# Performance work log

Measured on AMD Instinct MI355X. Metric: run time of the kernel, lower is better.

Reference implementation:

```python
import jax, jax.numpy as jnp
import numpy as np

B, T, I, H = 512, 1024, 64, 128

def setup_inputs() -> dict:
    key = jax.random.key(0)
    ks = jax.random.split(key, 7)
    s_ih = 1.0 / np.sqrt(H)  # torch nn.RNN init scale (uniform +-1/sqrt(H)); use scaled normal for stability
    return {
        "x": jax.random.normal(ks[0], (B, T, I), dtype=jnp.float32),
        "W_ih": jax.random.uniform(ks[1], (H, I), minval=-s_ih, maxval=s_ih, dtype=jnp.float32),
        "W_hh": jax.random.uniform(ks[2], (H, H), minval=-s_ih, maxval=s_ih, dtype=jnp.float32),
        "b_ih": jax.random.uniform(ks[3], (H,), minval=-s_ih, maxval=s_ih, dtype=jnp.float32),
        "b_hh": jax.random.uniform(ks[4], (H,), minval=-s_ih, maxval=s_ih, dtype=jnp.float32),
        "fc_w": jax.random.uniform(ks[5], (1, H), minval=-s_ih, maxval=s_ih, dtype=jnp.float32),
        "fc_b": jax.random.uniform(ks[6], (1,), minval=-s_ih, maxval=s_ih, dtype=jnp.float32),
    }

def reference(x, W_ih, W_hh, b_ih, b_hh, fc_w, fc_b):
    # Precompute input projection for all timesteps in one big GEMM: [B,T,H]
    xp = jnp.einsum("bti,hi->bth", x, W_ih) + b_ih + b_hh
    h0 = jnp.zeros((x.shape[0], W_hh.shape[0]), dtype=x.dtype)

    def step(h, xp_t):
        h = jnp.tanh(xp_t + h @ W_hh.T)
        return h, None

    # scan over time axis; only the final hidden state is needed (out[:, -1, :])
    h_last, _ = jax.lax.scan(step, h0, jnp.swapaxes(xp, 0, 1))
    out = h_last @ fc_w.T + fc_b  # [B, 1]
    return jax.nn.sigmoid(out)
```

## Files before the change

### kernel.cpp

```cpp
#include <hip/hip_runtime.h>


#define Bsz 512
#define Tt  1024
#define Ii  64
#define Hh  128
constexpr int TC = 32;
constexpr int NT = 256;

typedef _Float16 half2v __attribute__((ext_vector_type(2)));
typedef _Float16 half4v __attribute__((ext_vector_type(4)));
typedef _Float16 half8v __attribute__((ext_vector_type(8)));

union h8u { half8v v; half2v h[4]; };

__device__ __forceinline__ float dot2(half2v a, half2v b, float c) {
#if __has_builtin(__builtin_amdgcn_fdot2)
    return __builtin_amdgcn_fdot2(a, b, c, false);
#else
    return c + (float)a[0] * (float)b[0] + (float)a[1] * (float)b[1];
#endif
}

__device__ __forceinline__ float fast_tanh(float x) {
    float t = __builtin_amdgcn_exp2f(x * 2.8853900817779268f);
    return 1.0f - 2.0f * __builtin_amdgcn_rcpf(t + 1.0f);
}
__device__ __forceinline__ float fast_sigmoid(float z) {
    float t = __builtin_amdgcn_exp2f(-z * 1.4426950408889634f);
    return __builtin_amdgcn_rcpf(1.0f + t);
}
__device__ __forceinline__ half4v cvt4(float4 p) {
    half4v r; r[0] = (_Float16)p.x; r[1] = (_Float16)p.y;
    r[2] = (_Float16)p.z; r[3] = (_Float16)p.w; return r;
}

__global__ __launch_bounds__(NT, 4)
void rnn_fused(const float* __restrict__ x,
               const float* __restrict__ W_ih,
               const float* __restrict__ W_hh,
               const float* __restrict__ b_ih,
               const float* __restrict__ b_hh,
               const float* __restrict__ fc_w,
               const float* __restrict__ fc_b,
               float* __restrict__ out)
{
    __shared__ __align__(16) _Float16 xs[2][TC * Ii];
    __shared__ __align__(16) _Float16 hbuf[2][Hh];
    __shared__ float wred[NT / 64];

    const int tid = threadIdx.x;
    const int kq  = tid & 3;
    const int jg  = tid >> 2;
    const int j0  = jg * 2, j1 = j0 + 1;
    const int row = blockIdx.x;

    half2v wih0[8], wih1[8];
    {
        const float* g0 = W_ih + j0 * Ii + kq * 16;
        const float* g1 = W_ih + j1 * Ii + kq * 16;
        #pragma unroll
        for (int k = 0; k < 8; ++k) {
            wih0[k][0] = (_Float16)g0[2*k]; wih0[k][1] = (_Float16)g0[2*k+1];
            wih1[k][0] = (_Float16)g1[2*k]; wih1[k][1] = (_Float16)g1[2*k+1];
        }
    }
    half2v whh0[16], whh1[16];
    {
        const float* g0 = W_hh + j0 * Hh + kq * 32;
        const float* g1 = W_hh + j1 * Hh + kq * 32;
        #pragma unroll
        for (int k = 0; k < 16; ++k) {
            whh0[k][0] = (_Float16)g0[2*k]; whh0[k][1] = (_Float16)g0[2*k+1];
            whh1[k][0] = (_Float16)g1[2*k]; whh1[k][1] = (_Float16)g1[2*k+1];
        }
    }
    const float bias0 = b_ih[j0] + b_hh[j0];
    const float bias1 = b_ih[j1] + b_hh[j1];
    const float fw0 = fc_w[j0], fw1 = fc_w[j1];

    if (tid < Hh / 2) ((half2v*)hbuf[0])[tid] = (half2v)0;

    const float4* xsrc = (const float4*)(x + (size_t)row * Tt * Ii);
    float4 p0 = xsrc[tid];
    float4 p1 = xsrc[tid + NT];

    int   cur = 0;
    float h0n = 0.0f, h1n = 0.0f;

    for (int t0 = 0; t0 < Tt; t0 += TC) {
        const int cbuf = (t0 / TC) & 1;
        ((half4v*)xs[cbuf])[tid]      = cvt4(p0);
        ((half4v*)xs[cbuf])[tid + NT] = cvt4(p1);
        if (t0 + TC < Tt) {
            const int base = (t0 + TC) * (Ii / 4);
            p0 = xsrc[base + tid];
            p1 = xsrc[base + tid + NT];
        }
        __syncthreads();

        #pragma unroll 2
        for (int tt = 0; tt < TC; ++tt) {
            const half8v* xv = (const half8v*)(xs[cbuf] + tt * Ii) + kq * 2;
            const half8v* hv = (const half8v*)(hbuf[cur]) + kq * 4;
            h8u xq0, xq1, hq0, hq1, hq2, hq3;
            xq0.v = xv[0]; xq1.v = xv[1];
            hq0.v = hv[0]; hq1.v = hv[1];
            hq2.v = hv[2]; hq3.v = hv[3];

            float a0 = 0.f, a1 = 0.f, a2 = 0.f, a3 = 0.f;
            float c0 = 0.f, c1 = 0.f, c2 = 0.f, c3 = 0.f;
            #pragma unroll
            for (int k = 0; k < 4; ++k) {
                half2v u0 = xq0.h[k], u1 = xq1.h[k];
                a0 = dot2(u0, wih0[k],     a0);
                a1 = dot2(u1, wih0[k + 4], a1);
                c0 = dot2(u0, wih1[k],     c0);
                c1 = dot2(u1, wih1[k + 4], c1);
            }
            #pragma unroll
            for (int k = 0; k < 4; ++k) {
                half2v v0 = hq0.h[k], v1 = hq1.h[k];
                half2v v2 = hq2.h[k], v3 = hq3.h[k];
                a0 = dot2(v0, whh0[k],      a0);
                a1 = dot2(v1, whh0[k + 4],  a1);
                a2 = dot2(v2, whh0[k + 8],  a2);
                a3 = dot2(v3, whh0[k + 12], a3);
                c0 = dot2(v0, whh1[k],      c0);
                c1 = dot2(v1, whh1[k + 4],  c1);
                c2 = dot2(v2, whh1[k + 8],  c2);
                c3 = dot2(v3, whh1[k + 12], c3);
            }
            float pp0 = (a0 + a1) + (a2 + a3);
            float pp1 = (c0 + c1) + (c2 + c3);
            pp0 += __shfl_xor(pp0, 1, 64);
            pp0 += __shfl_xor(pp0, 2, 64);
            pp1 += __shfl_xor(pp1, 1, 64);
            pp1 += __shfl_xor(pp1, 2, 64);
            h0n = fast_tanh(pp0 + bias0);
            h1n = fast_tanh(pp1 + bias1);
            if (kq == 0) {
                half2v hw; hw[0] = (_Float16)h0n; hw[1] = (_Float16)h1n;
                ((half2v*)hbuf[cur ^ 1])[jg] = hw;
            }
            __syncthreads();
            cur ^= 1;
        }
    }

    float partial = (kq == 0) ? (fw0 * h0n + fw1 * h1n) : 0.0f;
    #pragma unroll
    for (int off = 32; off > 0; off >>= 1)
        partial += __shfl_down(partial, off, 64);
    if ((tid & 63) == 0) wred[tid >> 6] = partial;
    __syncthreads();
    if (tid == 0) {
        float z = fc_b[0];
        #pragma unroll
        for (int w = 0; w < NT / 64; ++w) z += wred[w];
        out[row] = fast_sigmoid(z);
    }
}

extern "C" void kernel_launch(void* const* d_in, const int* in_sizes, int n_in,
                              void* d_out, int out_size, void* d_ws, size_t ws_size,
                              hipStream_t stream) {
    const float* x    = (const float*)d_in[0];
    const float* W_ih = (const float*)d_in[1];
    const float* W_hh = (const float*)d_in[2];
    const float* b_ih = (const float*)d_in[3];
    const float* b_hh = (const float*)d_in[4];
    const float* fc_w = (const float*)d_in[5];
    const float* fc_b = (const float*)d_in[6];
    float* out = (float*)d_out;

    rnn_fused<<<Bsz, NT, 0, stream>>>(x, W_ih, W_hh, b_ih, b_hh, fc_w, fc_b, out);
}
```

Before: 625.3 us.

## Process two batch rows per block and precompute next-step input projection off critical path

Each block now runs two independent sequences at once, so every per-timestep barrier and shuffle reduction is shared across two rows and there is more independent work between syncs. The input projection for step t+1 is computed after the hidden-state write and before the barrier, taking it off the h-dependent critical path. Grid size halves to 256 blocks with launch bounds lowered to 2. That lowers parallelism across CUs and may increase register pressure.

```diff
diff --git a/kernel.cpp b/kernel.cpp
--- a/kernel.cpp
+++ b/kernel.cpp
@@ -5,8 +5,9 @@
 #define Tt  1024
 #define Ii  64
 #define Hh  128
-constexpr int TC = 32;
-constexpr int NT = 256;
+constexpr int TC  = 32;
+constexpr int NT  = 256;
+constexpr int RPB = 2;
 
 typedef _Float16 half2v __attribute__((ext_vector_type(2)));
 typedef _Float16 half4v __attribute__((ext_vector_type(4)));
@@ -35,25 +36,26 @@
     r[2] = (_Float16)p.z; r[3] = (_Float16)p.w; return r;
 }
 
-__global__ __launch_bounds__(NT, 4)
-void rnn_fused(const float* __restrict__ x,
-               const float* __restrict__ W_ih,
-               const float* __restrict__ W_hh,
-               const float* __restrict__ b_ih,
-               const float* __restrict__ b_hh,
-               const float* __restrict__ fc_w,
-               const float* __restrict__ fc_b,
-               float* __restrict__ out)
+__global__ __launch_bounds__(NT, 2)
+void rnn_fused2(const float* __restrict__ x,
+                const float* __restrict__ W_ih,
+                const float* __restrict__ W_hh,
+                const float* __restrict__ b_ih,
+                const float* __restrict__ b_hh,
+                const float* __restrict__ fc_w,
+                const float* __restrict__ fc_b,
+                float* __restrict__ out)
 {
-    __shared__ __align__(16) _Float16 xs[2][TC * Ii];
-    __shared__ __align__(16) _Float16 hbuf[2][Hh];
-    __shared__ float wred[NT / 64];
+    __shared__ __align__(16) _Float16 xsh[2][RPB][TC * Ii];
+    __shared__ __align__(16) _Float16 hbuf[2][RPB][Hh];
+    __shared__ float wred[RPB][NT / 64];
 
     const int tid = threadIdx.x;
     const int kq  = tid & 3;
     const int jg  = tid >> 2;
     const int j0  = jg * 2, j1 = j0 + 1;
-    const int row = blockIdx.x;
+    const int rowA = blockIdx.x * RPB;
+    const int rowB = rowA + 1;
 
     half2v wih0[8], wih1[8];
     {
@@ -79,86 +81,121 @@
     const float bias1 = b_ih[j1] + b_hh[j1];
     const float fw0 = fc_w[j0], fw1 = fc_w[j1];
 
-    if (tid < Hh / 2) ((half2v*)hbuf[0])[tid] = (half2v)0;
-
-    const float4* xsrc = (const float4*)(x + (size_t)row * Tt * Ii);
-    float4 p0 = xsrc[tid];
-    float4 p1 = xsrc[tid + NT];
-
-    int   cur = 0;
-    float h0n = 0.0f, h1n = 0.0f;
+    if (tid < RPB * Hh / 2) ((half2v*)hbuf[0])[tid] = (half2v)0;
+
+    const float4* xgA = (const float4*)(x + (size_t)rowA * Tt * Ii);
+    const float4* xgB = (const float4*)(x + (size_t)rowB * Tt * Ii);
+    float4 pA0 = xgA[tid], pA1 = xgA[tid + NT];
+    float4 pB0 = xgB[tid], pB1 = xgB[tid + NT];
+
+    float hA0 = 0.f, hA1 = 0.f, hB0 = 0.f, hB1 = 0.f;
+    float fxA0, fxA1, fxA2, fxA3, fxB0, fxB1, fxB2, fxB3;
+
+#define XDOT(TTv, CBv)                                                       \
+    do {                                                                     \
+        const half8v* xvA = (const half8v*)(xsh[CBv][0] + (TTv) * Ii) + kq*2;\
+        const half8v* xvB = (const half8v*)(xsh[CBv][1] + (TTv) * Ii) + kq*2;\
+        h8u xa0, xa1, xb0, xb1;                                              \
+        xa0.v = xvA[0]; xa1.v = xvA[1];                                      \
+        xb0.v = xvB[0]; xb1.v = xvB[1];                                      \
+        fxA0 = 0.f; fxA1 = 0.f; fxA2 = 0.f; fxA3 = 0.f;                      \
+        fxB0 = 0.f; fxB1 = 0.f; fxB2 = 0.f; fxB3 = 0.f;                      \
+        _Pragma("unroll")                                                    \
+        for (int k = 0; k < 4; ++k) {                                        \
+            fxA0 = dot2(xa0.h[k], wih0[k],     fxA0);                        \
+            fxA1 = dot2(xa1.h[k], wih0[k + 4], fxA1);                        \
+            fxA2 = dot2(xa0.h[k], wih1[k],     fxA2);                        \
+            fxA3 = dot2(xa1.h[k], wih1[k + 4], fxA3);                        \
+            fxB0 = dot2(xb0.h[k], wih0[k],     fxB0);                        \
+            fxB1 = dot2(xb1.h[k], wih0[k + 4], fxB1);                        \
+            fxB2 = dot2(xb0.h[k], wih1[k],     fxB2);                        \
+            fxB3 = dot2(xb1.h[k], wih1[k + 4], fxB3);                        \
+        }                                                                    \
+    } while (0)
 
     for (int t0 = 0; t0 < Tt; t0 += TC) {
-        const int cbuf = (t0 / TC) & 1;
-        ((half4v*)xs[cbuf])[tid]      = cvt4(p0);
-        ((half4v*)xs[cbuf])[tid + NT] = cvt4(p1);
+        const int cb = (t0 / TC) & 1;
+        ((half4v*)xsh[cb][0])[tid]      = cvt4(pA0);
+        ((half4v*)xsh[cb][0])[tid + NT] = cvt4(pA1);
+        ((half4v*)xsh[cb][1])[tid]      = cvt4(pB0);
+        ((half4v*)xsh[cb][1])[tid + NT] = cvt4(pB1);
         if (t0 + TC < Tt) {
             const int base = (t0 + TC) * (Ii / 4);
-            p0 = xsrc[base + tid];
-            p1 = xsrc[base + tid + NT];
+            pA0 = xgA[base + tid]; pA1 = xgA[base + tid + NT];
+            pB0 = xgB[base + tid]; pB1 = xgB[base + tid + NT];
         }
         __syncthreads();
+        XDOT(0, cb);
 
         #pragma unroll 2
         for (int tt = 0; tt < TC; ++tt) {
-            const half8v* xv = (const half8v*)(xs[cbuf] + tt * Ii) + kq * 2;
-            const half8v* hv = (const half8v*)(hbuf[cur]) + kq * 4;
-            h8u xq0, xq1, hq0, hq1, hq2, hq3;
-            xq0.v = xv[0]; xq1.v = xv[1];
-            hq0.v = hv[0]; hq1.v = hv[1];
-            hq2.v = hv[2]; hq3.v = hv[3];
-
-            float a0 = 0.f, a1 = 0.f, a2 = 0.f, a3 = 0.f;
-            float c0 = 0.f, c1 = 0.f, c2 = 0.f, c3 = 0.f;
+            const int hb = tt & 1;
+            const half8v* hvA = (const half8v*)(hbuf[hb][0]) + kq * 4;
+            const half8v* hvB = (const half8v*)(hbuf[hb][1]) + kq * 4;
+            h8u ha0, ha1, ha2, ha3, hbq0, hbq1, hbq2, hbq3;
+            ha0.v = hvA[0]; ha1.v = hvA[1]; ha2.v = hvA[2]; ha3.v = hvA[3];
+            hbq0.v = hvB[0]; hbq1.v = hvB[1]; hbq2.v = hvB[2]; hbq3.v = hvB[3];
+
+            float aA0 = fxA0, aA1 = fxA1, aA2 = 0.f, aA3 = 0.f;
+            float cA0 = fxA2, cA1 = fxA3, cA2 = 0.f, cA3 = 0.f;
+            float aB0 = fxB0, aB1 = fxB1, aB2 = 0.f, aB3 = 0.f;
+            float cB0 = fxB2, cB1 = fxB3, cB2 = 0.f, cB3 = 0.f;
             #pragma unroll
             for (int k = 0; k < 4; ++k) {
-                half2v u0 = xq0.h[k], u1 = xq1.h[k];
-                a0 = dot2(u0, wih0[k],     a0);
-                a1 = dot2(u1, wih0[k + 4], a1);
-                c0 = dot2(u0, wih1[k],     c0);
-                c1 = dot2(u1, wih1[k + 4], c1);
+                aA0 = dot2(ha0.h[k], whh0[k],      aA0);
+                aA1 = dot2(ha1.h[k], whh0[k + 4],  aA1);
+                aA2 = dot2(ha2.h[k], whh0[k + 8],  aA2);
+                aA3 = dot2(ha3.h[k], whh0[k + 12], aA3);
+                cA0 = dot2(ha0.h[k], whh1[k],      cA0);
+                cA1 = dot2(ha1.h[k], whh1[k + 4],  cA1);
+                cA2 = dot2(ha2.h[k], whh1[k + 8],  cA2);
+                cA3 = dot2(ha3.h[k], whh1[k + 12], cA3);
+                aB0 = dot2(hbq0.h[k], whh0[k],      aB0);
+                aB1 = dot2(hbq1.h[k], whh0[k + 4],  aB1);
+                aB2 = dot2(hbq2.h[k], whh0[k + 8],  aB2);
+                aB3 = dot2(hbq3.h[k], whh0[k + 12], aB3);
+                cB0 = dot2(hbq0.h[k], whh1[k],      cB0);
+                cB1 = dot2(hbq1.h[k], whh1[k + 4],  cB1);
+                cB2 = dot2(hbq2.h[k], whh1[k + 8],  cB2);
+                cB3 = dot2(hbq3.h[k], whh1[k + 12], cB3);
             }
-            #pragma unroll
-            for (int k = 0; k < 4; ++k) {
-                half2v v0 = hq0.h[k], v1 = hq1.h[k];
-                half2v v2 = hq2.h[k], v3 = hq3.h[k];
-                a0 = dot2(v0, whh0[k],      a0);
-                a1 = dot2(v1, whh0[k + 4],  a1);
-                a2 = dot2(v2, whh0[k + 8],  a2);
-                a3 = dot2(v3, whh0[k + 12], a3);
-                c0 = dot2(v0, whh1[k],      c0);
-                c1 = dot2(v1, whh1[k + 4],  c1);
-                c2 = dot2(v2, whh1[k + 8],  c2);
-                c3 = dot2(v3, whh1[k + 12], c3);
+            float ppA0 = (aA0 + aA1) + (aA2 + aA3);
+            float ppA1 = (cA0 + cA1) + (cA2 + cA3);
+            float ppB0 = (aB0 + aB1) + (aB2 + aB3);
+            float ppB1 = (cB0 + cB1) + (cB2 + cB3);
+            ppA0 += __shfl_xor(ppA0, 1, 64); ppA0 += __shfl_xor(ppA0, 2, 64);
+            ppA1 += __shfl_xor(ppA1, 1, 64); ppA1 += __shfl_xor(ppA1, 2, 64);
+            ppB0 += __shfl_xor(ppB0, 1, 64); ppB0 += __shfl_xor(ppB0, 2, 64);
+            ppB1 += __shfl_xor(ppB1, 1, 64); ppB1 += __shfl_xor(ppB1, 2, 64);
+            hA0 = fast_tanh(ppA0 + bias0);
+            hA1 = fast_tanh(ppA1 + bias1);
+            hB0 = fast_tanh(ppB0 + bias0);
+            hB1 = fast_tanh(ppB1 + bias1);
+            if (kq == 0) {
+                half2v wA; wA[0] = (_Float16)hA0; wA[1] = (_Float16)hA1;
+                half2v wB; wB[0] = (_Float16)hB0; wB[1] = (_Float16)hB1;
+                ((half2v*)hbuf[hb ^ 1][0])[jg] = wA;
+                ((half2v*)hbuf[hb ^ 1][1])[jg] = wB;
             }
-            float pp0 = (a0 + a1) + (a2 + a3);
-            float pp1 = (c0 + c1) + (c2 + c3);
-            pp0 += __shfl_xor(pp0, 1, 64);
-            pp0 += __shfl_xor(pp0, 2, 64);
-            pp1 += __shfl_xor(pp1, 1, 64);
-            pp1 += __shfl_xor(pp1, 2, 64);
-            h0n = fast_tanh(pp0 + bias0);
-            h1n = fast_tanh(pp1 + bias1);
-            if (kq == 0) {
-                half2v hw; hw[0] = (_Float16)h0n; hw[1] = (_Float16)h1n;
-                ((half2v*)hbuf[cur ^ 1])[jg] = hw;
-            }
+            if (tt != TC - 1) XDOT(tt + 1, cb);
             __syncthreads();
-            cur ^= 1;
-        }
-    }
-
-    float partial = (kq == 0) ? (fw0 * h0n + fw1 * h1n) : 0.0f;
+        }
+    }
+
+    float pA = (kq == 0) ? (fw0 * hA0 + fw1 * hA1) : 0.0f;
+    float pB = (kq == 0) ? (fw0 * hB0 + fw1 * hB1) : 0.0f;
     #pragma unroll
-    for (int off = 32; off > 0; off >>= 1)
-        partial += __shfl_down(partial, off, 64);
-    if ((tid & 63) == 0) wred[tid >> 6] = partial;
+    for (int off = 32; off > 0; off >>= 1) {
+        pA += __shfl_down(pA, off, 64);
+        pB += __shfl_down(pB, off, 64);
+    }
+    if ((tid & 63) == 0) { wred[0][tid >> 6] = pA; wred[1][tid >> 6] = pB; }
     __syncthreads();
-    if (tid == 0) {
+    if (tid < RPB) {
         float z = fc_b[0];
         #pragma unroll
-        for (int w = 0; w < NT / 64; ++w) z += wred[w];
-        out[row] = fast_sigmoid(z);
+        for (int w = 0; w < NT / 64; ++w) z += wred[tid][w];
+        out[rowA + tid] = fast_sigmoid(z);
     }
 }
 
@@ -174,5 +211,5 @@
     const float* fc_b = (const float*)d_in[6];
     float* out = (float*)d_out;
 
-    rnn_fused<<<Bsz, NT, 0, stream>>>(x, W_ih, W_hh, b_ih, b_hh, fc_w, fc_b, out);
-}
+    rnn_fused2<<<Bsz / RPB, NT, 0, stream>>>(x, W_ih, W_hh, b_ih, b_hh, fc_w, fc_b, out);
+}
```

Result: slower. 715.5 us (+14.4%).

## Assign one hidden unit per thread and precompute next input projection early

Applied to the files above, without the earlier changes.

Each block now uses 128 threads, one per hidden unit. Each thread keeps a full W_hh row and W_ih row in registers, which removes the cross-lane shuffle reduction on every timestep. The input projection for step t+1 is computed after writing h and before the barrier, taking it off the serial dependency chain. In exchange each thread carries far more registers (96 half2 weights) and does more sequential dot products, and every thread reads the whole h vector from LDS each step. Occupancy bounds are lowered to match.

```diff
diff --git a/kernel.cpp b/kernel.cpp
--- a/kernel.cpp
+++ b/kernel.cpp
@@ -6,7 +6,7 @@
 #define Ii  64
 #define Hh  128
 constexpr int TC = 32;
-constexpr int NT = 256;
+constexpr int NT = 128;
 
 typedef _Float16 half2v __attribute__((ext_vector_type(2)));
 typedef _Float16 half4v __attribute__((ext_vector_type(4)));
@@ -35,131 +35,120 @@
     r[2] = (_Float16)p.z; r[3] = (_Float16)p.w; return r;
 }
 
-__global__ __launch_bounds__(NT, 4)
-void rnn_fused(const float* __restrict__ x,
-               const float* __restrict__ W_ih,
-               const float* __restrict__ W_hh,
-               const float* __restrict__ b_ih,
-               const float* __restrict__ b_hh,
-               const float* __restrict__ fc_w,
-               const float* __restrict__ fc_b,
-               float* __restrict__ out)
+__global__ __launch_bounds__(NT, 2)
+void rnn_rowwave(const float* __restrict__ x,
+                 const float* __restrict__ W_ih,
+                 const float* __restrict__ W_hh,
+                 const float* __restrict__ b_ih,
+                 const float* __restrict__ b_hh,
+                 const float* __restrict__ fc_w,
+                 const float* __restrict__ fc_b,
+                 float* __restrict__ out)
 {
     __shared__ __align__(16) _Float16 xs[2][TC * Ii];
-    __shared__ __align__(16) _Float16 hbuf[2][Hh];
-    __shared__ float wred[NT / 64];
+    __shared__ __align__(16) _Float16 hb[2][Hh];
+    __shared__ float wred[2];
 
     const int tid = threadIdx.x;
-    const int kq  = tid & 3;
-    const int jg  = tid >> 2;
-    const int j0  = jg * 2, j1 = j0 + 1;
     const int row = blockIdx.x;
 
-    half2v wih0[8], wih1[8];
+    half2v whh[64];
     {
-        const float* g0 = W_ih + j0 * Ii + kq * 16;
-        const float* g1 = W_ih + j1 * Ii + kq * 16;
+        const float4* g = (const float4*)(W_hh + tid * Hh);
         #pragma unroll
-        for (int k = 0; k < 8; ++k) {
-            wih0[k][0] = (_Float16)g0[2*k]; wih0[k][1] = (_Float16)g0[2*k+1];
-            wih1[k][0] = (_Float16)g1[2*k]; wih1[k][1] = (_Float16)g1[2*k+1];
+        for (int k = 0; k < 32; ++k) {
+            float4 v = g[k];
+            whh[2*k][0]   = (_Float16)v.x; whh[2*k][1]   = (_Float16)v.y;
+            whh[2*k+1][0] = (_Float16)v.z; whh[2*k+1][1] = (_Float16)v.w;
         }
     }
-    half2v whh0[16], whh1[16];
+    half2v wih[32];
     {
-        const float* g0 = W_hh + j0 * Hh + kq * 32;
-        const float* g1 = W_hh + j1 * Hh + kq * 32;
+        const float4* g = (const float4*)(W_ih + tid * Ii);
         #pragma unroll
         for (int k = 0; k < 16; ++k) {
-            whh0[k][0] = (_Float16)g0[2*k]; whh0[k][1] = (_Float16)g0[2*k+1];
-            whh1[k][0] = (_Float16)g1[2*k]; whh1[k][1] = (_Float16)g1[2*k+1];
+            float4 v = g[k];
+            wih[2*k][0]   = (_Float16)v.x; wih[2*k][1]   = (_Float16)v.y;
+            wih[2*k+1][0] = (_Float16)v.z; wih[2*k+1][1] = (_Float16)v.w;
         }
     }
-    const float bias0 = b_ih[j0] + b_hh[j0];
-    const float bias1 = b_ih[j1] + b_hh[j1];
-    const float fw0 = fc_w[j0], fw1 = fc_w[j1];
+    const float bias = b_ih[tid] + b_hh[tid];
+    const float fw   = fc_w[tid];
 
-    if (tid < Hh / 2) ((half2v*)hbuf[0])[tid] = (half2v)0;
+    if (tid < Hh / 2) ((half2v*)hb[0])[tid] = (half2v)0;
 
     const float4* xsrc = (const float4*)(x + (size_t)row * Tt * Ii);
-    float4 p0 = xsrc[tid];
-    float4 p1 = xsrc[tid + NT];
+    float4 p0 = xsrc[tid], p1 = xsrc[tid + NT], p2 = xsrc[tid + 2*NT], p3 = xsrc[tid + 3*NT];
 
-    int   cur = 0;
-    float h0n = 0.0f, h1n = 0.0f;
+    float hn = 0.0f;
+    float fx0, fx1, fx2, fx3;
+
+#define XP(TTv, CBv)                                                         \
+    do {                                                                     \
+        const h8u* xv = (const h8u*)(xs[CBv] + (TTv) * Ii);                  \
+        fx0 = 0.f; fx1 = 0.f; fx2 = 0.f; fx3 = 0.f;                          \
+        _Pragma("unroll")                                                    \
+        for (int k = 0; k < 8; ++k) {                                        \
+            h8u xq; xq.v = xv[k].v;                                          \
+            fx0 = dot2(xq.h[0], wih[4*k    ], fx0);                          \
+            fx1 = dot2(xq.h[1], wih[4*k + 1], fx1);                          \
+            fx2 = dot2(xq.h[2], wih[4*k + 2], fx2);                          \
+            fx3 = dot2(xq.h[3], wih[4*k + 3], fx3);                          \
+        }                                                                    \
+    } while (0)
 
     for (int t0 = 0; t0 < Tt; t0 += TC) {
-        const int cbuf = (t0 / TC) & 1;
-        ((half4v*)xs[cbuf])[tid]      = cvt4(p0);
-        ((half4v*)xs[cbuf])[tid + NT] = cvt4(p1);
+        const int cb = (t0 / TC) & 1;
+        ((half4v*)xs[cb])[tid]          = cvt4(p0);
+        ((half4v*)xs[cb])[tid + NT]     = cvt4(p1);
+        ((half4v*)xs[cb])[tid + 2*NT]   = cvt4(p2);
+        ((half4v*)xs[cb])[tid + 3*NT]   = cvt4(p3);
         if (t0 + TC < Tt) {
             const int base = (t0 + TC) * (Ii / 4);
-            p0 = xsrc[base + tid];
-            p1 = xsrc[base + tid + NT];
+            p0 = xsrc[base + tid];        p1 = xsrc[base + tid + NT];
+            p2 = xsrc[base + tid + 2*NT]; p3 = xsrc[base + tid + 3*NT];
         }
         __syncthreads();
+        XP(0, cb);
 
         #pragma unroll 2
         for (int tt = 0; tt < TC; ++tt) {
-            const half8v* xv = (const half8v*)(xs[cbuf] + tt * Ii) + kq * 2;
-            const half8v* hv = (const half8v*)(hbuf[cur]) + kq * 4;
-            h8u xq0, xq1, hq0, hq1, hq2, hq3;
-            xq0.v = xv[0]; xq1.v = xv[1];
-            hq0.v = hv[0]; hq1.v = hv[1];
-            hq2.v = hv[2]; hq3.v = hv[3];
-
-            float a0 = 0.f, a1 = 0.f, a2 = 0.f, a3 = 0.f;
-            float c0 = 0.f, c1 = 0.f, c2 = 0.f, c3 = 0.f;
+            const int p = tt & 1;
+            const h8u* hv = (const h8u*)(hb[p]);
+            float a0 = fx0, a1 = fx1, a2 = fx2, a3 = fx3;
+            float a4 = 0.f, a5 = 0.f, a6 = 0.f, a7 = 0.f;
             #pragma unroll
-            for (int k = 0; k < 4; ++k) {
-                half2v u0 = xq0.h[k], u1 = xq1.h[k];
-                a0 = dot2(u0, wih0[k],     a0);
-                a1 = dot2(u1, wih0[k + 4], a1);
-                c0 = dot2(u0, wih1[k],     c0);
-                c1 = dot2(u1, wih1[k + 4], c1);
+            for (int k = 0; k < 16; ++k) {
+                h8u hq; hq.v = hv[k].v;
+                const int c = (k & 1) * 4;
+                if (c == 0) {
+                    a0 = dot2(hq.h[0], whh[4*k    ], a0);
+                    a1 = dot2(hq.h[1], whh[4*k + 1], a1);
+                    a2 = dot2(hq.h[2], whh[4*k + 2], a2);
+                    a3 = dot2(hq.h[3], whh[4*k + 3], a3);
+                } else {
+                    a4 = dot2(hq.h[0], whh[4*k    ], a4);
+                    a5 = dot2(hq.h[1], whh[4*k + 1], a5);
+                    a6 = dot2(hq.h[2], whh[4*k + 2], a6);
+                    a7 = dot2(hq.h[3], whh[4*k + 3], a7);
+                }
             }
-            #pragma unroll
-            for (int k = 0; k < 4; ++k) {
-                half2v v0 = hq0.h[k], v1 = hq1.h[k];
-                half2v v2 = hq2.h[k], v3 = hq3.h[k];
-                a0 = dot2(v0, whh0[k],      a0);
-                a1 = dot2(v1, whh0[k + 4],  a1);
-                a2 = dot2(v2, whh0[k + 8],  a2);
-                a3 = dot2(v3, whh0[k + 12], a3);
-                c0 = dot2(v0, whh1[k],      c0);
-                c1 = dot2(v1, whh1[k + 4],  c1);
-                c2 = dot2(v2, whh1[k + 8],  c2);
-                c3 = dot2(v3, whh1[k + 12], c3);
-            }
-            float pp0 = (a0 + a1) + (a2 + a3);
-            float pp1 = (c0 + c1) + (c2 + c3);
-            pp0 += __shfl_xor(pp0, 1, 64);
-            pp0 += __shfl_xor(pp0, 2, 64);
-            pp1 += __shfl_xor(pp1, 1, 64);
-            pp1 += __shfl_xor(pp1, 2, 64);
-            h0n = fast_tanh(pp0 + bias0);
-            h1n = fast_tanh(pp1 + bias1);
-            if (kq == 0) {
-                half2v hw; hw[0] = (_Float16)h0n; hw[1] = (_Float16)h1n;
-                ((half2v*)hbuf[cur ^ 1])[jg] = hw;
-            }
+            float s = ((a0 + a1) + (a2 + a3)) + ((a4 + a5) + (a6 + a7));
+            hn = fast_tanh(s + bias);
+            ((_Float16*)hb[p ^ 1])[tid] = (_Float16)hn;
+            if (tt != TC - 1) XP(tt + 1, cb);
             __syncthreads();
-            cur ^= 1;
         }
     }
 
-    float partial = (kq == 0) ? (fw0 * h0n + fw1 * h1n) : 0.0f;
+    float partial = fw * hn;
     #pragma unroll
     for (int off = 32; off > 0; off >>= 1)
         partial += __shfl_down(partial, off, 64);
     if ((tid & 63) == 0) wred[tid >> 6] = partial;
     __syncthreads();
-    if (tid == 0) {
-        float z = fc_b[0];
-        #pragma unroll
-        for (int w = 0; w < NT / 64; ++w) z += wred[w];
-        out[row] = fast_sigmoid(z);
-    }
+    if (tid == 0)
+        out[row] = fast_sigmoid(fc_b[0] + wred[0] + wred[1]);
 }
 
 extern "C" void kernel_launch(void* const* d_in, const int* in_sizes, int n_in,
@@ -174,5 +163,5 @@
     const float* fc_b = (const float*)d_in[6];
     float* out = (float*)d_out;
 
-    rnn_fused<<<Bsz, NT, 0, stream>>>(x, W_ih, W_hh, b_ih, b_hh, fc_w, fc_b, out);
+    rnn_rowwave<<<Bsz, NT, 0, stream>>>(x, W_ih, W_hh, b_ih, b_hh, fc_w, fc_b, out);
 }
```

New measurement: 787.0 us. 1.26x slower.
